# Performance work log

Measured on AMD Instinct MI355X. Metric: run time of the kernel, lower is better.

Reference implementation:

```python
import jax, jax.numpy as jnp
import numpy as np

B = 1024          # batch_size from init
TEMP = 0.5        # temperature buffer
EPS_NORM = 1e-12  # F.normalize eps
EPS_COS = 1e-8    # F.cosine_similarity eps


def setup_inputs() -> dict:
    key = jax.random.key(0)
    k1, k2 = jax.random.split(key)
    emb_i = jax.random.normal(k1, (B, 128, 128), dtype=jnp.float32)
    emb_j = jax.random.normal(k2, (B, 128, 128), dtype=jnp.float32)
    return {"emb_i": emb_i, "emb_j": emb_j}


def reference(emb_i, emb_j):
    # F.normalize(x, dim=1): L2-normalize over the m axis of [B, m, n]
    def norm_dim1(x):
        n = jnp.sqrt(jnp.sum(x * x, axis=1, keepdims=True))
        return x / jnp.maximum(n, EPS_NORM)

    z_i = norm_dim1(emb_i)
    z_j = norm_dim1(emb_j)
    reps = jnp.concatenate([z_i, z_j], axis=0)        # [2B, m, n]
    flat = reps.reshape(2 * B, -1)                    # [2B, D]

    # cosine similarity of flattened vectors == matmul of re-normalized rows
    rn = flat / jnp.maximum(
        jnp.sqrt(jnp.sum(flat * flat, axis=1, keepdims=True)), EPS_COS)
    sim = rn @ rn.T                                   # [2B, 2B]

    sim_ij = jnp.diagonal(sim, offset=B)              # [B]
    sim_ji = jnp.diagonal(sim, offset=-B)             # [B]
    positives = jnp.concatenate([sim_ij, sim_ji], axis=0)  # [2B]

    negatives_mask = 1.0 - jnp.eye(2 * B, dtype=sim.dtype)
    nominator = jnp.exp(positives / TEMP)
    denominator = jnp.sum(negatives_mask * jnp.exp(sim / TEMP), axis=1)
    loss_partial = -jnp.log(nominator / denominator)
    return jnp.sum(loss_partial) / (2 * B)
```

## Files before the change

kernel.cpp:

```cpp
#include <hip/hip_runtime.h>
#include <hip/hip_bf16.h>
#include <math.h>

#define B_SZ   1024
#define NROW   2048
#define D_K    16384
#define SPLIT  8
#define KSEG   (D_K / SPLIT)
#define NTILE  16
#define NPAIR  136
#define TEMP_SIM (2.0f / 256.0f)

typedef float f32x4 __attribute__((ext_vector_type(4)));
typedef long  i64;

typedef __attribute__((address_space(1))) unsigned int GU32;
typedef __attribute__((address_space(3))) unsigned int LU32;

__device__ __forceinline__ void async16(const void* g, void* l) {
  __builtin_amdgcn_global_load_lds((GU32*)(g), (LU32*)(l), 16, 0, 0);
}

__global__ __launch_bounds__(512) void norm_kernel(
    const float* __restrict__ emb_i, const float* __restrict__ emb_j,
    unsigned char* __restrict__ rn, float* __restrict__ sim,
    float* __restrict__ rsum, unsigned int* __restrict__ cnt)
{
  const int b = blockIdx.x;
  const int t = threadIdx.x;
  const int c = t & 31;
  const int g = t >> 5;

  ((f32x4*)sim)[(size_t)b * 512 + t] = (f32x4){0.f, 0.f, 0.f, 0.f};
  if (b == 0) {
    for (int k = t; k < NROW; k += 512) rsum[k] = 0.f;
    if (t == 0) *cnt = 0u;
  }

  const float* src = (b < B_SZ) ? (emb_i + (size_t)b * D_K)
                                : (emb_j + (size_t)(b - B_SZ) * D_K);

  f32x4 vals[8];
  f32x4 ss = (f32x4){0.f, 0.f, 0.f, 0.f};
#pragma unroll
  for (int mm = 0; mm < 8; ++mm) {
    f32x4 v = *(const f32x4*)(src + (size_t)(g * 8 + mm) * 128 + c * 4);
    vals[mm] = v;
    ss += v * v;
  }

  __shared__ f32x4 part[16][32];
  part[g][c] = ss;
  __syncthreads();
  f32x4 css = part[0][c];
#pragma unroll
  for (int gg = 1; gg < 16; ++gg) css += part[gg][c];

  f32x4 mcn, colz2;
#pragma unroll
  for (int k = 0; k < 4; ++k) {
    mcn[k] = fmaxf(sqrtf(css[k]), 1e-12f);
    colz2[k] = css[k] / (mcn[k] * mcn[k]);
  }
  float s = colz2[0] + colz2[1] + colz2[2] + colz2[3];
#pragma unroll
  for (int off = 1; off < 64; off <<= 1) s += __shfl_xor(s, off);
  const float rowfac = fmaxf(sqrtf(0.5f * s), 1e-8f);

  f32x4 scale;
#pragma unroll
  for (int k = 0; k < 4; ++k) scale[k] = 16.0f / (mcn[k] * rowfac);

  unsigned char* dst = rn + (size_t)b * D_K;
#pragma unroll
  for (int mm = 0; mm < 8; ++mm) {
    f32x4 sv = vals[mm] * scale;
    int p = 0;
    p = __builtin_amdgcn_cvt_pk_fp8_f32(sv[0], sv[1], p, false);
    p = __builtin_amdgcn_cvt_pk_fp8_f32(sv[2], sv[3], p, true);
    *(int*)(dst + (size_t)(g * 8 + mm) * 128 + c * 4) = p;
  }
}

__global__ __launch_bounds__(256) void gemm_sim_kernel(
    const unsigned char* __restrict__ rn, float* __restrict__ sim)
{
  int idx = blockIdx.y, tI = 0, rem = NTILE;
  while (idx >= rem) { idx -= rem; --rem; ++tI; }
  const int tJ = tI + idx;
  const bool diag = (tI == tJ);

  const int kBase = blockIdx.x * KSEG;
  const int t    = threadIdx.x;
  const int lane = t & 63;
  const int wave = t >> 6;
  const int wm = wave >> 1, wn = wave & 1;
  const int quad = lane >> 4, col = lane & 15;

  __shared__ __align__(16) unsigned char As[2][128 * 32];
  __shared__ __align__(16) unsigned char Bs[2][128 * 32];

  const unsigned char* aG = rn + (size_t)(tI * 128 + (t >> 1)) * D_K + kBase + (t & 1) * 16;
  const unsigned char* bG = rn + (size_t)(tJ * 128 + (t >> 1)) * D_K + kBase + (t & 1) * 16;
  unsigned char* aL0 = &As[0][t * 16];
  unsigned char* aL1 = &As[1][t * 16];
  unsigned char* bL0 = &Bs[0][t * 16];
  unsigned char* bL1 = &Bs[1][t * 16];

  f32x4 acc[4][4];
#pragma unroll
  for (int mi = 0; mi < 4; ++mi)
#pragma unroll
    for (int ni = 0; ni < 4; ++ni)
      acc[mi][ni] = (f32x4){0.f, 0.f, 0.f, 0.f};

  const int aOff = (wm * 64 + col) * 32 + quad * 8;
  const int bOff = (wn * 64 + col) * 32 + quad * 8;

  for (int k0 = 0; k0 < KSEG; k0 += 64) {
    __syncthreads();
    async16(aG + k0,      aL0);
    async16(aG + k0 + 32, aL1);
    async16(bG + k0,      bL0);
    async16(bG + k0 + 32, bL1);
    __syncthreads();

#pragma unroll
    for (int h = 0; h < 2; ++h) {
      i64 af[4], bf[4];
#pragma unroll
      for (int mi = 0; mi < 4; ++mi) af[mi] = *(const i64*)(&As[h][aOff + mi * 16 * 32]);
#pragma unroll
      for (int ni = 0; ni < 4; ++ni) bf[ni] = *(const i64*)(&Bs[h][bOff + ni * 16 * 32]);
#pragma unroll
      for (int mi = 0; mi < 4; ++mi)
#pragma unroll
        for (int ni = 0; ni < 4; ++ni)
          acc[mi][ni] = __builtin_amdgcn_mfma_f32_16x16x32_fp8_fp8(
              af[mi], bf[ni], acc[mi][ni], 0, 0, 0);
    }
  }

  const int iB = tI * 128 + wm * 64;
  const int jB = tJ * 128 + wn * 64;
#pragma unroll
  for (int mi = 0; mi < 4; ++mi) {
#pragma unroll
    for (int reg = 0; reg < 4; ++reg) {
      const int i = iB + mi * 16 + quad * 4 + reg;
#pragma unroll
      for (int ni = 0; ni < 4; ++ni) {
        const int j = jB + ni * 16 + col;
        if (!diag || j >= i)
          atomicAdd(&sim[(size_t)i * NROW + j], acc[mi][ni][reg]);
      }
    }
  }
}

__global__ __launch_bounds__(256) void loss_tile_kernel(
    const float* __restrict__ sim, float* __restrict__ rsum,
    unsigned int* __restrict__ cnt, float* __restrict__ out)
{
  int idx = blockIdx.x, tI = 0, rem = NTILE;
  while (idx >= rem) { idx -= rem; --rem; ++tI; }
  const int tJ = tI + idx;
  const bool diag = (tI == tJ);

  const int t   = threadIdx.x;
  const int w   = t >> 6;
  const int l   = t & 63;
  const int hf  = l >> 5;
  const int sub = l & 31;
  const int jb  = tJ * 128 + sub * 4;

  float ca[4] = {0.f, 0.f, 0.f, 0.f};

#pragma unroll
  for (int step = 0; step < 16; ++step) {
    const int r  = w * 32 + step * 2 + hf;
    const int gi = tI * 128 + r;
    f32x4 v = *(const f32x4*)(sim + (size_t)gi * NROW + jb);
    float e[4];
#pragma unroll
    for (int k = 0; k < 4; ++k) {
      e[k] = __expf(TEMP_SIM * v[k]);
      if (diag && (jb + k <= gi)) e[k] = 0.f;
      ca[k] += e[k];
    }
    float rp = e[0] + e[1] + e[2] + e[3];
#pragma unroll
    for (int off = 1; off < 32; off <<= 1) rp += __shfl_xor(rp, off);
    if (sub == 0) atomicAdd(&rsum[gi], rp);
  }

  __shared__ float colacc[8][128];
#pragma unroll
  for (int k = 0; k < 4; ++k) colacc[w * 2 + hf][sub * 4 + k] = ca[k];
  __syncthreads();
  if (t < 128) {
    float s = 0.f;
#pragma unroll
    for (int q = 0; q < 8; ++q) s += colacc[q][t];
    atomicAdd(&rsum[tJ * 128 + t], s);
  }

  __syncthreads();
  __shared__ bool last;
  if (t == 0) {
    __threadfence();
    last = (atomicAdd(cnt, 1u) == NPAIR - 1);
  }
  __syncthreads();
  if (!last) return;

  float s = 0.f;
  for (int i = t; i < NROW; i += 256) {
    const int jp = (i < B_SZ) ? i + B_SZ : i - B_SZ;
    const float pos = (jp >= i) ? sim[(size_t)i * NROW + jp]
                                : sim[(size_t)jp * NROW + i];
    const float rs = atomicAdd(&rsum[i], 0.f);
    s += logf(rs) - TEMP_SIM * pos;
  }
#pragma unroll
  for (int off = 1; off < 64; off <<= 1) s += __shfl_xor(s, off);
  __shared__ float r[4];
  if ((t & 63) == 0) r[t >> 6] = s;
  __syncthreads();
  if (t == 0) out[0] = (r[0] + r[1] + r[2] + r[3]) * (1.0f / NROW);
}

extern "C" void kernel_launch(void* const* d_in, const int* in_sizes, int n_in,
                              void* d_out, int out_size, void* d_ws, size_t ws_size,
                              hipStream_t stream) {
  const float* emb_i = (const float*)d_in[0];
  const float* emb_j = (const float*)d_in[1];
  float* out = (float*)d_out;

  char* ws = (char*)d_ws;
  unsigned char* rn = (unsigned char*)ws;
  float* sim  = (float*)(ws + (size_t)NROW * D_K);
  float* rsum = sim + (size_t)NROW * NROW;
  unsigned int* cnt = (unsigned int*)(rsum + NROW);

  norm_kernel<<<dim3(NROW), dim3(512), 0, stream>>>(emb_i, emb_j, rn, sim, rsum, cnt);
  gemm_sim_kernel<<<dim3(SPLIT, NPAIR), dim3(256), 0, stream>>>(rn, sim);
  loss_tile_kernel<<<dim3(NPAIR), dim3(256), 0, stream>>>(sim, rsum, cnt, out);
}
```

Measured before the change: 286.4 us.

## Give each wave its own 64x64 tile with per-wave double-buffered LDS pipeline

Retiles the fp8 similarity GEMM so each wave independently computes a 64x64 upper-triangle tile pair. Each wave uses private double-buffered LDS staging with an XOR swizzle and explicit waitcnt instead of block-wide barriers. This is meant to overlap global-to-LDS loads with MFMA work, remove __syncthreads stalls, and reduce LDS bank conflicts. The cost is smaller tiles with less data reuse, so more global/L2 traffic per FLOP.

```diff
diff --git a/kernel.cpp b/kernel.cpp
--- a/kernel.cpp
+++ b/kernel.cpp
@@ -7,6 +7,8 @@
 #define D_K    16384
 #define SPLIT  8
 #define KSEG   (D_K / SPLIT)
+#define NT64   32
+#define NPAIR64 528
 #define NTILE  16
 #define NPAIR  136
 #define TEMP_SIM (2.0f / 256.0f)
@@ -85,27 +87,27 @@
 __global__ __launch_bounds__(256) void gemm_sim_kernel(
     const unsigned char* __restrict__ rn, float* __restrict__ sim)
 {
-  int idx = blockIdx.y, tI = 0, rem = NTILE;
+  const int t    = threadIdx.x;
+  const int lane = t & 63;
+  const int wave = t >> 6;
+  const int quad = lane >> 4, col = lane & 15;
+
+  int idx = blockIdx.y * 4 + wave, tI = 0, rem = NT64;
   while (idx >= rem) { idx -= rem; --rem; ++tI; }
   const int tJ = tI + idx;
   const bool diag = (tI == tJ);
 
   const int kBase = blockIdx.x * KSEG;
-  const int t    = threadIdx.x;
-  const int lane = t & 63;
-  const int wave = t >> 6;
-  const int wm = wave >> 1, wn = wave & 1;
-  const int quad = lane >> 4, col = lane & 15;
-
-  __shared__ __align__(16) unsigned char As[2][128 * 32];
-  __shared__ __align__(16) unsigned char Bs[2][128 * 32];
-
-  const unsigned char* aG = rn + (size_t)(tI * 128 + (t >> 1)) * D_K + kBase + (t & 1) * 16;
-  const unsigned char* bG = rn + (size_t)(tJ * 128 + (t >> 1)) * D_K + kBase + (t & 1) * 16;
-  unsigned char* aL0 = &As[0][t * 16];
-  unsigned char* aL1 = &As[1][t * 16];
-  unsigned char* bL0 = &Bs[0][t * 16];
-  unsigned char* bL1 = &Bs[1][t * 16];
+
+  __shared__ __align__(16) unsigned char LA[2][4][2048];
+  __shared__ __align__(16) unsigned char LB[2][4][2048];
+
+  const int srow = lane >> 1;
+  const int c16  = (lane & 1) ^ ((srow >> 2) & 1);
+  const unsigned char* aG0 = rn + (size_t)(tI * 64 + srow)      * D_K + kBase + c16 * 16;
+  const unsigned char* aG1 = rn + (size_t)(tI * 64 + 32 + srow) * D_K + kBase + c16 * 16;
+  const unsigned char* bG0 = rn + (size_t)(tJ * 64 + srow)      * D_K + kBase + c16 * 16;
+  const unsigned char* bG1 = rn + (size_t)(tJ * 64 + 32 + srow) * D_K + kBase + c16 * 16;
 
   f32x4 acc[4][4];
 #pragma unroll
@@ -114,35 +116,58 @@
     for (int ni = 0; ni < 4; ++ni)
       acc[mi][ni] = (f32x4){0.f, 0.f, 0.f, 0.f};
 
-  const int aOff = (wm * 64 + col) * 32 + quad * 8;
-  const int bOff = (wn * 64 + col) * 32 + quad * 8;
-
-  for (int k0 = 0; k0 < KSEG; k0 += 64) {
-    __syncthreads();
-    async16(aG + k0,      aL0);
-    async16(aG + k0 + 32, aL1);
-    async16(bG + k0,      bL0);
-    async16(bG + k0 + 32, bL1);
-    __syncthreads();
-
-#pragma unroll
-    for (int h = 0; h < 2; ++h) {
-      i64 af[4], bf[4];
-#pragma unroll
-      for (int mi = 0; mi < 4; ++mi) af[mi] = *(const i64*)(&As[h][aOff + mi * 16 * 32]);
-#pragma unroll
-      for (int ni = 0; ni < 4; ++ni) bf[ni] = *(const i64*)(&Bs[h][bOff + ni * 16 * 32]);
-#pragma unroll
-      for (int mi = 0; mi < 4; ++mi)
-#pragma unroll
-        for (int ni = 0; ni < 4; ++ni)
-          acc[mi][ni] = __builtin_amdgcn_mfma_f32_16x16x32_fp8_fp8(
-              af[mi], bf[ni], acc[mi][ni], 0, 0, 0);
+  const int c2 = (col >> 2) & 1;
+  const int pw = ((quad >> 1) ^ c2) * 16 + (quad & 1) * 8;
+
+  const int NIT = KSEG / 32;
+
+  {
+    unsigned char* la = &LA[0][wave][lane * 16];
+    unsigned char* lb = &LB[0][wave][lane * 16];
+    async16(aG0, la);
+    async16(aG1, la + 1024);
+    async16(bG0, lb);
+    async16(bG1, lb + 1024);
+  }
+
+  for (int it = 0; it < NIT; ++it) {
+    const int buf = it & 1;
+    __builtin_amdgcn_sched_barrier(0);
+    if (it + 1 < NIT) {
+      const int k1 = (it + 1) * 32;
+      unsigned char* la = &LA[buf ^ 1][wave][lane * 16];
+      unsigned char* lb = &LB[buf ^ 1][wave][lane * 16];
+      async16(aG0 + k1, la);
+      async16(aG1 + k1, la + 1024);
+      async16(bG0 + k1, lb);
+      async16(bG1 + k1, lb + 1024);
+      __builtin_amdgcn_sched_barrier(0);
+      __builtin_amdgcn_s_waitcnt(0x0F74);
+    } else {
+      __builtin_amdgcn_sched_barrier(0);
+      __builtin_amdgcn_s_waitcnt(0x0F70);
     }
-  }
-
-  const int iB = tI * 128 + wm * 64;
-  const int jB = tJ * 128 + wn * 64;
+    __builtin_amdgcn_sched_barrier(0);
+
+    const unsigned char* pa = &LA[buf][wave][0];
+    const unsigned char* pb = &LB[buf][wave][0];
+    i64 af[4], bf[4];
+#pragma unroll
+    for (int mi = 0; mi < 4; ++mi)
+      af[mi] = *(const i64*)(pa + (mi * 16 + col) * 32 + pw);
+#pragma unroll
+    for (int ni = 0; ni < 4; ++ni)
+      bf[ni] = *(const i64*)(pb + (ni * 16 + col) * 32 + pw);
+#pragma unroll
+    for (int mi = 0; mi < 4; ++mi)
+#pragma unroll
+      for (int ni = 0; ni < 4; ++ni)
+        acc[mi][ni] = __builtin_amdgcn_mfma_f32_16x16x32_fp8_fp8(
+            af[mi], bf[ni], acc[mi][ni], 0, 0, 0);
+  }
+
+  const int iB = tI * 64;
+  const int jB = tJ * 64;
 #pragma unroll
   for (int mi = 0; mi < 4; ++mi) {
 #pragma unroll
@@ -244,6 +269,6 @@
   unsigned int* cnt = (unsigned int*)(rsum + NROW);
 
   norm_kernel<<<dim3(NROW), dim3(512), 0, stream>>>(emb_i, emb_j, rn, sim, rsum, cnt);
-  gemm_sim_kernel<<<dim3(SPLIT, NPAIR), dim3(256), 0, stream>>>(rn, sim);
+  gemm_sim_kernel<<<dim3(SPLIT, NPAIR64 / 4), dim3(256), 0, stream>>>(rn, sim);
   loss_tile_kernel<<<dim3(NPAIR), dim3(256), 0, stream>>>(sim, rsum, cnt, out);
 }
```

New measurement: 316.7 us. 1.11x slower.

## Widen GEMM K-step to 128 with XOR-swizzled row-major LDS tiles

Applied to the files above, without the earlier changes.

The fp8 GEMM now stages a 128x128-byte K-slab per operand per iteration instead of two 32-byte halves. Each row's 16-byte chunks are placed with an XOR swizzle on the row index to avoid LDS bank conflicts on the MFMA fragment reads. This halves the number of barrier pairs per K segment and gives each global load a full 128-byte row segment for better coalescing. The cost is 32KB of LDS per block, which may lower occupancy, and there is still no double buffering to overlap loads with compute.

```diff
diff --git a/kernel.cpp b/kernel.cpp
--- a/kernel.cpp
+++ b/kernel.cpp
@@ -97,15 +97,13 @@
   const int wm = wave >> 1, wn = wave & 1;
   const int quad = lane >> 4, col = lane & 15;
 
-  __shared__ __align__(16) unsigned char As[2][128 * 32];
-  __shared__ __align__(16) unsigned char Bs[2][128 * 32];
-
-  const unsigned char* aG = rn + (size_t)(tI * 128 + (t >> 1)) * D_K + kBase + (t & 1) * 16;
-  const unsigned char* bG = rn + (size_t)(tJ * 128 + (t >> 1)) * D_K + kBase + (t & 1) * 16;
-  unsigned char* aL0 = &As[0][t * 16];
-  unsigned char* aL1 = &As[1][t * 16];
-  unsigned char* bL0 = &Bs[0][t * 16];
-  unsigned char* bL1 = &Bs[1][t * 16];
+  __shared__ __align__(16) unsigned char As[128 * 128];
+  __shared__ __align__(16) unsigned char Bs[128 * 128];
+
+  const int srow = t >> 3;
+  const int gc   = (t & 7) ^ (srow & 7);
+  const unsigned char* aGb = rn + (size_t)(tI * 128 + srow) * D_K + kBase + gc * 16;
+  const unsigned char* bGb = rn + (size_t)(tJ * 128 + srow) * D_K + kBase + gc * 16;
 
   f32x4 acc[4][4];
 #pragma unroll
@@ -114,24 +112,25 @@
     for (int ni = 0; ni < 4; ++ni)
       acc[mi][ni] = (f32x4){0.f, 0.f, 0.f, 0.f};
 
-  const int aOff = (wm * 64 + col) * 32 + quad * 8;
-  const int bOff = (wn * 64 + col) * 32 + quad * 8;
-
-  for (int k0 = 0; k0 < KSEG; k0 += 64) {
+  for (int k0 = 0; k0 < KSEG; k0 += 128) {
     __syncthreads();
-    async16(aG + k0,      aL0);
-    async16(aG + k0 + 32, aL1);
-    async16(bG + k0,      bL0);
-    async16(bG + k0 + 32, bL1);
+#pragma unroll
+    for (int i = 0; i < 4; ++i) {
+      async16(aGb + (size_t)(32 * i) * D_K + k0, &As[i * 4096 + t * 16]);
+      async16(bGb + (size_t)(32 * i) * D_K + k0, &Bs[i * 4096 + t * 16]);
+    }
     __syncthreads();
 
 #pragma unroll
-    for (int h = 0; h < 2; ++h) {
+    for (int h = 0; h < 4; ++h) {
+      const int off = ((2 * h + (quad >> 1)) ^ (col & 7)) * 16 + (quad & 1) * 8;
       i64 af[4], bf[4];
 #pragma unroll
-      for (int mi = 0; mi < 4; ++mi) af[mi] = *(const i64*)(&As[h][aOff + mi * 16 * 32]);
-#pragma unroll
-      for (int ni = 0; ni < 4; ++ni) bf[ni] = *(const i64*)(&Bs[h][bOff + ni * 16 * 32]);
+      for (int mi = 0; mi < 4; ++mi)
+        af[mi] = *(const i64*)(&As[(wm * 64 + mi * 16 + col) * 128 + off]);
+#pragma unroll
+      for (int ni = 0; ni < 4; ++ni)
+        bf[ni] = *(const i64*)(&Bs[(wn * 64 + ni * 16 + col) * 128 + off]);
 #pragma unroll
       for (int mi = 0; mi < 4; ++mi)
 #pragma unroll
```

Measured after the change: 259.4 us. 9.4% less time.
